# Performance work log

Measured on AMD Instinct MI355X. Metric: run time of the kernel, lower is better.

Reference implementation:

```python
import jax, jax.numpy as jnp
import numpy as np

DN = ('NCHW', 'OIHW', 'NCHW')  # dimension numbers for all convs


def _dwconv(x, w, dim):
    # depthwise conv, valid padding; w: (dim,1,kh,kw)
    return jax.lax.conv_general_dilated(
        x, w, window_strides=(1, 1), padding='VALID',
        dimension_numbers=DN, feature_group_count=dim)


def setup_inputs() -> dict:
    key = jax.random.key(0)
    ks = jax.random.split(key, 5)
    B, C, H, W = 16, 256, 96, 96
    REP_K = 3
    x = jax.random.normal(ks[0], (B, C, H, W), dtype=jnp.float32)
    meta_pe = jax.random.normal(ks[1], (1, C, H, 1), dtype=jnp.float32) * 0.02
    weight = jax.random.normal(ks[2], (C, 1, H, 1), dtype=jnp.float32) * 0.02
    bias = jnp.zeros((C,), dtype=jnp.float32)
    rep_weight = jax.random.normal(ks[3], (C, 1, REP_K, 1), dtype=jnp.float32) * 0.02
    return {'x': x, 'meta_pe': meta_pe, 'weight': weight, 'bias': bias,
            'rep_weight': rep_weight}


def reference(x, meta_pe, weight, bias, rep_weight):
    # type == 'H': circular padding / conv along the H axis (kernels (K,1))
    dim = x.shape[1]
    rep_k = rep_weight.shape[2]
    # positional embedding add (broadcast over batch and W)
    x = x + meta_pe
    # local branch: circular pad by rep_k-1 rows, small depthwise conv
    x_cat = jnp.concatenate([x, x[:, :, :rep_k - 1, :]], axis=2)
    x_rep = _dwconv(x_cat, rep_weight, dim)
    # global branch: circular pad by H-1 rows, full-height depthwise conv + bias
    x_cat = jnp.concatenate([x, x[:, :, :-1, :]], axis=2)
    x_gcc = _dwconv(x_cat, weight, dim) + bias[None, :, None, None]
    return x_rep + x_gcc
```

## Files before the change

kernel.cpp:

```cpp
#include <hip/hip_runtime.h>

#define B_   16
#define C_   256
#define HH   96
#define WW   96
#define TPB  64

typedef _Float16 half8 __attribute__((ext_vector_type(8)));
typedef float   f32x16 __attribute__((ext_vector_type(16)));

__global__ __launch_bounds__(TPB) void fused_circ_conv_mfma(
    const float* __restrict__ x,
    const float* __restrict__ meta_pe,
    const float* __restrict__ weight,
    const float* __restrict__ bias,
    const float* __restrict__ rep_weight,
    float* __restrict__ out)
{
    __shared__ __align__(16) float sX[HH][32];
    __shared__ float sW[2 * HH];

    const int lane = threadIdx.x;
    const int blk  = blockIdx.x;
    const int bc   = blk & (B_ * C_ - 1);
    const int s    = blk >> 12;
    const int c    = bc & (C_ - 1);
    const size_t base = (size_t)bc * (HH * WW);

    const int r32 = lane & 31;
    const int g   = lane >> 5;

#pragma unroll
    for (int t = 0; t < 3; ++t) {
        int u = lane + TPB * t;
        int k = (u < HH) ? u : u - HH;
        float w_ = weight[c * HH + k];
        if (k < 3) w_ += rep_weight[c * 3 + k];
        sW[u] = w_;
    }

    {
        const int q  = lane & 7;
        const int jr = lane >> 3;
        const float* __restrict__ xg = x + base + s * 32 + q * 4;
        const float* __restrict__ pe = meta_pe + c * HH;
#pragma unroll
        for (int t = 0; t < 12; ++t) {
            const int j = t * 8 + jr;
            float4 v = *(const float4*)(xg + (size_t)j * WW);
            float m = pe[j];
            v.x += m; v.y += m; v.z += m; v.w += m;
            *(float4*)(&sX[j][q * 4]) = v;
        }
    }
    __syncthreads();

    half8 ah[6], al[6], bh[6], bl[6];
#pragma unroll
    for (int t = 0; t < 6; ++t) {
        const float* wp = sW + (96 + t * 16 + g * 8 - r32);
#pragma unroll
        for (int e = 0; e < 8; ++e) {
            float w_ = wp[e];
            _Float16 h = (_Float16)w_;
            ah[t][e] = h;
            al[t][e] = (_Float16)(w_ - (float)h);
            float v = sX[t * 16 + g * 8 + e][r32];
            _Float16 hb = (_Float16)v;
            bh[t][e] = hb;
            bl[t][e] = (_Float16)(v - (float)hb);
        }
    }

    const float bv = bias[c];
    float* __restrict__ op = out + base + (s * 32 + r32);

#pragma unroll
    for (int m = 0; m < 3; ++m) {
        f32x16 acc;
#pragma unroll
        for (int i = 0; i < 16; ++i) acc[i] = 0.f;
#pragma unroll
        for (int kt = 0; kt < 6; ++kt) {
            const int t = (kt + 6 - 2 * m) % 6;
            acc = __builtin_amdgcn_mfma_f32_32x32x16_f16(ah[t], bh[kt], acc, 0, 0, 0);
            acc = __builtin_amdgcn_mfma_f32_32x32x16_f16(al[t], bh[kt], acc, 0, 0, 0);
            acc = __builtin_amdgcn_mfma_f32_32x32x16_f16(ah[t], bl[kt], acc, 0, 0, 0);
        }
#pragma unroll
        for (int reg = 0; reg < 16; ++reg) {
            int row = m * 32 + (reg & 3) + 8 * (reg >> 2) + 4 * g;
            op[(size_t)row * WW] = acc[reg] + bv;
        }
    }
}

extern "C" void kernel_launch(void* const* d_in, const int* in_sizes, int n_in,
                              void* d_out, int out_size, void* d_ws, size_t ws_size,
                              hipStream_t stream) {
    const float* x          = (const float*)d_in[0];
    const float* meta_pe    = (const float*)d_in[1];
    const float* weight     = (const float*)d_in[2];
    const float* bias       = (const float*)d_in[3];
    const float* rep_weight = (const float*)d_in[4];
    float* out = (float*)d_out;

    fused_circ_conv_mfma<<<dim3(3 * B_ * C_), dim3(TPB), 0, stream>>>(
        x, meta_pe, weight, bias, rep_weight, out);
}
```

Measured before the change: 278.3 us.

## Process four images per block, precompute meta_pe conv, prefetch x into registers

Each block now handles four batch images for one channel and column strip, so the split-fp16 weight fragments are built once and reused across images. The positional-embedding contribution is computed once per block with MFMA, since conv is linear and meta_pe is shared across batch. The result, plus bias, seeds the accumulators. Loads of x go straight from global memory into registers, skipping the LDS staging, and the next image is prefetched during the current image's MFMAs. The change cuts redundant weight conversion and LDS traffic but adds register pressure and reduces the grid to a quarter as many blocks.

```diff
diff --git a/kernel.cpp b/kernel.cpp
--- a/kernel.cpp
+++ b/kernel.cpp
@@ -4,6 +4,7 @@
 #define C_   256
 #define HH   96
 #define WW   96
+#define IMG  4
 #define TPB  64
 
 typedef _Float16 half8 __attribute__((ext_vector_type(8)));
@@ -17,15 +18,13 @@
     const float* __restrict__ rep_weight,
     float* __restrict__ out)
 {
-    __shared__ __align__(16) float sX[HH][32];
     __shared__ float sW[2 * HH];
 
     const int lane = threadIdx.x;
     const int blk  = blockIdx.x;
-    const int bc   = blk & (B_ * C_ - 1);
-    const int s    = blk >> 12;
-    const int c    = bc & (C_ - 1);
-    const size_t base = (size_t)bc * (HH * WW);
+    const int s    = blk >> 10;
+    const int c    = (blk & 1023) >> 2;
+    const int b0   = (blk & 3) * IMG;
 
     const int r32 = lane & 31;
     const int g   = lane >> 5;
@@ -38,24 +37,9 @@
         if (k < 3) w_ += rep_weight[c * 3 + k];
         sW[u] = w_;
     }
-
-    {
-        const int q  = lane & 7;
-        const int jr = lane >> 3;
-        const float* __restrict__ xg = x + base + s * 32 + q * 4;
-        const float* __restrict__ pe = meta_pe + c * HH;
-#pragma unroll
-        for (int t = 0; t < 12; ++t) {
-            const int j = t * 8 + jr;
-            float4 v = *(const float4*)(xg + (size_t)j * WW);
-            float m = pe[j];
-            v.x += m; v.y += m; v.z += m; v.w += m;
-            *(float4*)(&sX[j][q * 4]) = v;
-        }
-    }
     __syncthreads();
 
-    half8 ah[6], al[6], bh[6], bl[6];
+    half8 ah[6], al[6];
 #pragma unroll
     for (int t = 0; t < 6; ++t) {
         const float* wp = sW + (96 + t * 16 + g * 8 - r32);
@@ -65,32 +49,92 @@
             _Float16 h = (_Float16)w_;
             ah[t][e] = h;
             al[t][e] = (_Float16)(w_ - (float)h);
-            float v = sX[t * 16 + g * 8 + e][r32];
-            _Float16 hb = (_Float16)v;
-            bh[t][e] = hb;
-            bl[t][e] = (_Float16)(v - (float)hb);
         }
     }
 
     const float bv = bias[c];
-    float* __restrict__ op = out + base + (s * 32 + r32);
-
-#pragma unroll
-    for (int m = 0; m < 3; ++m) {
-        f32x16 acc;
-#pragma unroll
-        for (int i = 0; i < 16; ++i) acc[i] = 0.f;
+    f32x16 acc0[3];
+    {
+        half8 ph[6], pl[6];
+        const float* pep = meta_pe + c * HH + g * 8;
 #pragma unroll
         for (int kt = 0; kt < 6; ++kt) {
-            const int t = (kt + 6 - 2 * m) % 6;
-            acc = __builtin_amdgcn_mfma_f32_32x32x16_f16(ah[t], bh[kt], acc, 0, 0, 0);
-            acc = __builtin_amdgcn_mfma_f32_32x32x16_f16(al[t], bh[kt], acc, 0, 0, 0);
-            acc = __builtin_amdgcn_mfma_f32_32x32x16_f16(ah[t], bl[kt], acc, 0, 0, 0);
+#pragma unroll
+            for (int e = 0; e < 8; ++e) {
+                float v = pep[kt * 16 + e];
+                _Float16 h = (_Float16)v;
+                ph[kt][e] = h;
+                pl[kt][e] = (_Float16)(v - (float)h);
+            }
         }
 #pragma unroll
-        for (int reg = 0; reg < 16; ++reg) {
-            int row = m * 32 + (reg & 3) + 8 * (reg >> 2) + 4 * g;
-            op[(size_t)row * WW] = acc[reg] + bv;
+        for (int m = 0; m < 3; ++m) {
+            f32x16 a;
+#pragma unroll
+            for (int i = 0; i < 16; ++i) a[i] = bv;
+#pragma unroll
+            for (int kt = 0; kt < 6; ++kt) {
+                const int t = (kt + 6 - 2 * m) % 6;
+                a = __builtin_amdgcn_mfma_f32_32x32x16_f16(ah[t], ph[kt], a, 0, 0, 0);
+                a = __builtin_amdgcn_mfma_f32_32x32x16_f16(al[t], ph[kt], a, 0, 0, 0);
+                a = __builtin_amdgcn_mfma_f32_32x32x16_f16(ah[t], pl[kt], a, 0, 0, 0);
+            }
+            acc0[m] = a;
+        }
+    }
+
+    const int col = s * 32 + r32;
+    const size_t IMGSTR = (size_t)C_ * HH * WW;
+    const size_t base0  = (size_t)(b0 * C_ + c) * (HH * WW);
+    const float* __restrict__ xl = x + base0 + (size_t)(g * 8) * WW + col;
+    float* __restrict__ ol = out + base0 + col;
+
+    float bx[48];
+#pragma unroll
+    for (int kt = 0; kt < 6; ++kt)
+#pragma unroll
+        for (int e = 0; e < 8; ++e)
+            bx[kt * 8 + e] = xl[(size_t)(kt * 16 + e) * WW];
+
+#pragma unroll 1
+    for (int img = 0; img < IMG; ++img) {
+        half8 bh[6], bl[6];
+#pragma unroll
+        for (int kt = 0; kt < 6; ++kt)
+#pragma unroll
+            for (int e = 0; e < 8; ++e) {
+                float v = bx[kt * 8 + e];
+                _Float16 h = (_Float16)v;
+                bh[kt][e] = h;
+                bl[kt][e] = (_Float16)(v - (float)h);
+            }
+        __builtin_amdgcn_sched_barrier(0);
+        if (img + 1 < IMG) {
+            const float* __restrict__ xn = xl + (size_t)(img + 1) * IMGSTR;
+#pragma unroll
+            for (int kt = 0; kt < 6; ++kt)
+#pragma unroll
+                for (int e = 0; e < 8; ++e)
+                    bx[kt * 8 + e] = xn[(size_t)(kt * 16 + e) * WW];
+        }
+        __builtin_amdgcn_sched_barrier(0);
+
+        float* __restrict__ op = ol + (size_t)img * IMGSTR;
+#pragma unroll
+        for (int m = 0; m < 3; ++m) {
+            f32x16 acc = acc0[m];
+#pragma unroll
+            for (int kt = 0; kt < 6; ++kt) {
+                const int t = (kt + 6 - 2 * m) % 6;
+                acc = __builtin_amdgcn_mfma_f32_32x32x16_f16(ah[t], bh[kt], acc, 0, 0, 0);
+                acc = __builtin_amdgcn_mfma_f32_32x32x16_f16(al[t], bh[kt], acc, 0, 0, 0);
+                acc = __builtin_amdgcn_mfma_f32_32x32x16_f16(ah[t], bl[kt], acc, 0, 0, 0);
+            }
+#pragma unroll
+            for (int reg = 0; reg < 16; ++reg) {
+                int row = m * 32 + (reg & 3) + 8 * (reg >> 2) + 4 * g;
+                op[(size_t)row * WW] = acc[reg];
+            }
         }
     }
 }
@@ -105,6 +149,6 @@
     const float* rep_weight = (const float*)d_in[4];
     float* out = (float*)d_out;
 
-    fused_circ_conv_mfma<<<dim3(3 * B_ * C_), dim3(TPB), 0, stream>>>(
+    fused_circ_conv_mfma<<<dim3(3 * 1024), dim3(TPB), 0, stream>>>(
         x, meta_pe, weight, bias, rep_weight, out);
 }
```

New measurement: 280.1 us. About the same (+0.6%).
